# Kernel tuning notes

Hardware: AMD Instinct MI355X
Metric: run time of the kernel (lower is better)

Reference implementation:

```python
import jax, jax.numpy as jnp
import numpy as np

B, L, T = 256, 1024, 128


def setup_inputs() -> dict:
    key = jax.random.key(0)
    k1, k2, k3, k4 = jax.random.split(key, 4)
    inputs = jax.random.normal(k1, (B, L, T), dtype=jnp.float32)
    lengths = jax.random.randint(k2, (B,), 1, L + 1, dtype=jnp.int32)
    tags = jax.random.randint(k3, (B, L), 0, T, dtype=jnp.int32)
    # learned CRF transition matrix (random_normal_initializer default stddev=0.05)
    transition_params = jax.random.normal(k4, (T, T), dtype=jnp.float32) * 0.05
    return {"inputs": inputs, "lengths": lengths, "tags": tags,
            "transition_params": transition_params}


def _crf_decode(x, trans, lengths):
    """Viterbi decode. x: [B,L,T], trans: [T,T], lengths: [B] -> tags [B,L] int32."""
    Bx, Lx, Tx = x.shape

    def fwd_step(state, inp):
        x_t, t = inp  # x_t: [B,T]
        scores = state[:, :, None] + trans[None]          # [B, T_prev, T_cur]
        bp = jnp.argmax(scores, axis=1).astype(jnp.int32)  # [B,T]
        new_state = jnp.max(scores, axis=1) + x_t           # [B,T]
        m = (t < lengths)[:, None]
        state = jnp.where(m, new_state, state)
        bp = jnp.where(m, bp, 0)
        return state, bp

    init = x[:, 0]                                          # [B,T]
    xs = (jnp.swapaxes(x[:, 1:], 0, 1), jnp.arange(1, Lx))
    state, bps = jax.lax.scan(fwd_step, init, xs)           # bps: [L-1,B,T]
    bps = jnp.concatenate([jnp.zeros((1, Bx, Tx), jnp.int32), bps], axis=0)  # bp[0] unused
    last_tag = jnp.argmax(state, axis=-1).astype(jnp.int32)  # [B] tag at position length-1

    def bwd_step(carry, inp):
        bp_t, t = inp
        emit = jnp.where(t < lengths, carry, 0)             # tags beyond length -> 0
        prev = jnp.take_along_axis(bp_t, carry[:, None], axis=1)[:, 0]
        carry = jnp.where((t > 0) & (t < lengths), prev, carry)
        return carry, emit

    _, tags_rev = jax.lax.scan(bwd_step, last_tag, (bps[::-1], jnp.arange(Lx)[::-1]))
    return jnp.swapaxes(tags_rev[::-1], 0, 1)               # [B,L]


def reference(inputs, lengths, tags, transition_params):
    # Decoder.call: tfa.text.crf_decode(inputs, transition_params, lengths)[0]
    return _crf_decode(inputs, transition_params, lengths)
```

## Files before the change

kernel.cpp:

```cpp
#include <hip/hip_runtime.h>

#define BB 256
#define LL 1024
#define TT 128
#define NTH 512

__device__ __forceinline__ void lds_barrier() {
    asm volatile("s_waitcnt lgkmcnt(0)\n\ts_barrier" ::);
}

struct SmallSmem {
    float state[TT];
    float pv[NTH];
    int   pi[NTH];
    unsigned char tags[LL];
};

__global__ __launch_bounds__(NTH)
void viterbi_kernel(const float* __restrict__ x,
                    const int* __restrict__ lengths,
                    const float* __restrict__ trans,
                    int* __restrict__ out) {
    __shared__ SmallSmem sm;
    extern __shared__ unsigned char bp[];

    const int b   = blockIdx.x;
    const int tid = threadIdx.x;
    const int j   = tid & (TT - 1);
    const int q   = tid >> 7;

    int lenb = lengths[b];
    if (lenb < 1) lenb = 1;
    if (lenb > LL) lenb = LL;

    float tc[32];
    #pragma unroll
    for (int ii = 0; ii < 32; ++ii)
        tc[ii] = trans[(q * 32 + ii) * TT + j];

    const float* xb = x + (size_t)b * LL * TT;

    if (tid < TT) sm.state[tid] = xb[tid];

    float xv_cur = 0.0f, xv_next = 0.0f;
    if (tid < TT && lenb > 1) xv_cur = xb[TT + j];
    lds_barrier();

    for (int t = 1; t < lenb; ++t) {
        if (tid < TT) {
            int tn = (t + 1 < lenb) ? (t + 1) : (lenb - 1);
            xv_next = xb[tn * TT + j];
        }

        float best0 = -3.4e38f, best1 = -3.4e38f, best2 = -3.4e38f, best3 = -3.4e38f;
        int   bi0 = 0, bi1 = 1, bi2 = 2, bi3 = 3;
        const float4* st4 = reinterpret_cast<const float4*>(sm.state + q * 32);
        #pragma unroll
        for (int k = 0; k < 8; ++k) {
            float4 sv = st4[k];
            float s0 = sv.x + tc[4 * k + 0];
            float s1 = sv.y + tc[4 * k + 1];
            float s2 = sv.z + tc[4 * k + 2];
            float s3 = sv.w + tc[4 * k + 3];
            if (s0 > best0) { best0 = s0; bi0 = 4 * k + 0; }
            if (s1 > best1) { best1 = s1; bi1 = 4 * k + 1; }
            if (s2 > best2) { best2 = s2; bi2 = 4 * k + 2; }
            if (s3 > best3) { best3 = s3; bi3 = 4 * k + 3; }
        }
        float bb = best0; int bi = bi0;
        if (best1 > bb || (best1 == bb && bi1 < bi)) { bb = best1; bi = bi1; }
        if (best2 > bb || (best2 == bb && bi2 < bi)) { bb = best2; bi = bi2; }
        if (best3 > bb || (best3 == bb && bi3 < bi)) { bb = best3; bi = bi3; }
        sm.pv[tid] = bb;
        sm.pi[tid] = bi + q * 32;
        lds_barrier();

        if (tid < TT) {
            float bv = sm.pv[j];       int ix = sm.pi[j];
            float v1 = sm.pv[j + 128]; int i1 = sm.pi[j + 128];
            float v2 = sm.pv[j + 256]; int i2 = sm.pi[j + 256];
            float v3 = sm.pv[j + 384]; int i3 = sm.pi[j + 384];
            if (v1 > bv) { bv = v1; ix = i1; }
            if (v2 > bv) { bv = v2; ix = i2; }
            if (v3 > bv) { bv = v3; ix = i3; }
            sm.state[j] = bv + xv_cur;
            bp[t * TT + j] = (unsigned char)ix;
            xv_cur = xv_next;
        }
        lds_barrier();
    }

    if (tid == 0) {
        float bv = sm.state[0]; int ix = 0;
        for (int i = 1; i < TT; ++i) {
            float v = sm.state[i];
            if (v > bv) { bv = v; ix = i; }
        }
        int carry = ix;
        for (int t = lenb - 1; t >= 1; --t) {
            sm.tags[t] = (unsigned char)carry;
            carry = bp[t * TT + carry];
        }
        sm.tags[0] = (unsigned char)carry;
    }
    lds_barrier();

    int* outb = out + (size_t)b * LL;
    for (int t = tid; t < LL; t += NTH)
        outb[t] = (t < lenb) ? (int)sm.tags[t] : 0;
}

extern "C" void kernel_launch(void* const* d_in, const int* in_sizes, int n_in,
                              void* d_out, int out_size, void* d_ws, size_t ws_size,
                              hipStream_t stream) {
    const float* x       = (const float*)d_in[0];
    const int*   lengths = (const int*)d_in[1];
    const float* trans   = (const float*)d_in[3];
    int*         out     = (int*)d_out;

    const int dyn = LL * TT;
    hipFuncSetAttribute((const void*)&viterbi_kernel,
                        hipFuncAttributeMaxDynamicSharedMemorySize, dyn);
    viterbi_kernel<<<BB, NTH, dyn, stream>>>(x, lengths, trans, out);
}
```

Baseline: 934.1 us.

## Reduce Viterbi argmax across quad lanes with DPP and double-buffer state

Each output tag is now handled by four adjacent lanes, and their partial max/argmax results are combined with DPP quad permutes instead of going through shared memory. This removes one of the two block barriers per time step, along with the pv/pi shared-memory round trip. The state vector is double-buffered and padded so reads and writes of consecutive steps do not conflict. In exchange, every thread runs the shuffle compares, and the padded layout changes the LDS access pattern.

Result: slower. 984.3 us (+5.4%).

```diff
diff --git a/kernel.cpp b/kernel.cpp
--- a/kernel.cpp
+++ b/kernel.cpp
@@ -9,10 +9,21 @@
     asm volatile("s_waitcnt lgkmcnt(0)\n\ts_barrier" ::);
 }
 
-struct SmallSmem {
-    float state[TT];
-    float pv[NTH];
-    int   pi[NTH];
+template<int CTRL>
+__device__ __forceinline__ float dpp_f(float v) {
+    int r = __builtin_amdgcn_update_dpp(__float_as_int(v), __float_as_int(v),
+                                        CTRL, 0xF, 0xF, false);
+    return __int_as_float(r);
+}
+template<int CTRL>
+__device__ __forceinline__ int dpp_i(int v) {
+    return __builtin_amdgcn_update_dpp(v, v, CTRL, 0xF, 0xF, false);
+}
+
+#define SP(i) ((i) + (((i) >> 5) << 2))
+
+struct alignas(16) SmallSmem {
+    float st[2][144];
     unsigned char tags[LL];
 };
 
@@ -26,8 +37,8 @@
 
     const int b   = blockIdx.x;
     const int tid = threadIdx.x;
-    const int j   = tid & (TT - 1);
-    const int q   = tid >> 7;
+    const int j   = tid >> 2;
+    const int q   = tid & 3;
 
     int lenb = lengths[b];
     if (lenb < 1) lenb = 1;
@@ -40,21 +51,23 @@
 
     const float* xb = x + (size_t)b * LL * TT;
 
-    if (tid < TT) sm.state[tid] = xb[tid];
+    if (tid < TT) sm.st[0][SP(tid)] = xb[tid];
 
-    float xv_cur = 0.0f, xv_next = 0.0f;
-    if (tid < TT && lenb > 1) xv_cur = xb[TT + j];
+    float xv = 0.0f;
+    if (q == 0 && lenb > 1) xv = xb[TT + j];
     lds_barrier();
 
+    int p = 0;
     for (int t = 1; t < lenb; ++t) {
-        if (tid < TT) {
+        float xn = 0.0f;
+        if (q == 0) {
             int tn = (t + 1 < lenb) ? (t + 1) : (lenb - 1);
-            xv_next = xb[tn * TT + j];
+            xn = xb[tn * TT + j];
         }
 
+        const float4* st4 = reinterpret_cast<const float4*>(&sm.st[p][q * 36]);
         float best0 = -3.4e38f, best1 = -3.4e38f, best2 = -3.4e38f, best3 = -3.4e38f;
         int   bi0 = 0, bi1 = 1, bi2 = 2, bi3 = 3;
-        const float4* st4 = reinterpret_cast<const float4*>(sm.state + q * 32);
         #pragma unroll
         for (int k = 0; k < 8; ++k) {
             float4 sv = st4[k];
@@ -71,29 +84,30 @@
         if (best1 > bb || (best1 == bb && bi1 < bi)) { bb = best1; bi = bi1; }
         if (best2 > bb || (best2 == bb && bi2 < bi)) { bb = best2; bi = bi2; }
         if (best3 > bb || (best3 == bb && bi3 < bi)) { bb = best3; bi = bi3; }
-        sm.pv[tid] = bb;
-        sm.pi[tid] = bi + q * 32;
-        lds_barrier();
+        bi += q * 32;
 
-        if (tid < TT) {
-            float bv = sm.pv[j];       int ix = sm.pi[j];
-            float v1 = sm.pv[j + 128]; int i1 = sm.pi[j + 128];
-            float v2 = sm.pv[j + 256]; int i2 = sm.pi[j + 256];
-            float v3 = sm.pv[j + 384]; int i3 = sm.pi[j + 384];
-            if (v1 > bv) { bv = v1; ix = i1; }
-            if (v2 > bv) { bv = v2; ix = i2; }
-            if (v3 > bv) { bv = v3; ix = i3; }
-            sm.state[j] = bv + xv_cur;
-            bp[t * TT + j] = (unsigned char)ix;
-            xv_cur = xv_next;
+        {
+            float ov = dpp_f<0xB1>(bb);
+            int   oi = dpp_i<0xB1>(bi);
+            if (ov > bb || (ov == bb && oi < bi)) { bb = ov; bi = oi; }
+            ov = dpp_f<0x4E>(bb);
+            oi = dpp_i<0x4E>(bi);
+            if (ov > bb || (ov == bb && oi < bi)) { bb = ov; bi = oi; }
         }
+
+        if (q == 0) {
+            sm.st[p ^ 1][SP(j)] = bb + xv;
+            bp[t * TT + j] = (unsigned char)bi;
+            xv = xn;
+        }
+        p ^= 1;
         lds_barrier();
     }
 
     if (tid == 0) {
-        float bv = sm.state[0]; int ix = 0;
+        float bv = sm.st[p][SP(0)]; int ix = 0;
         for (int i = 1; i < TT; ++i) {
-            float v = sm.state[i];
+            float v = sm.st[p][SP(i)];
             if (v > bv) { bv = v; ix = i; }
         }
         int carry = ix;
```

## Drop argmax from forward pass; recover backpointers by recomputation during backtrace

Applied to the files above, without the earlier changes.

The forward Viterbi loop now computes only the max over previous states and writes each step's max value to a global workspace, so the per-step argmax bookkeeping and index reduction are gone. During backtrace, the chosen predecessor is found again by recomputing state+trans for the current tag and matching the stored max with a wavefront ballot. Workspace rows and inputs are staged into LDS in chunks. This adds a large global write stream (B*L*T floats) and a slower, serialized backward phase. Ties are resolved by taking the lowest matching index, and the recovered path relies on the recomputed float sums matching the stored maxima exactly.

Measured after the change: 776.1 us. -16.9%, faster.

```diff
diff --git a/kernel.cpp b/kernel.cpp
--- a/kernel.cpp
+++ b/kernel.cpp
@@ -4,9 +4,141 @@
 #define LL 1024
 #define TT 128
 #define NTH 512
+#define CH 64
+
+typedef unsigned long long ull;
 
 __device__ __forceinline__ void lds_barrier() {
     asm volatile("s_waitcnt lgkmcnt(0)\n\ts_barrier" ::);
+}
+
+struct FwdSmem {
+    float state[TT];
+    float pv[NTH];
+    unsigned char tags[LL];
+};
+
+__global__ __launch_bounds__(NTH)
+void viterbi_ws_kernel(const float* __restrict__ x,
+                       const int* __restrict__ lengths,
+                       const float* __restrict__ trans,
+                       int* __restrict__ out,
+                       float* __restrict__ ws) {
+    __shared__ FwdSmem sm;
+    extern __shared__ float dyn[];
+    float* tT = dyn;
+    float* bm = dyn + TT * TT;
+    float* bx = bm + CH * TT;
+
+    const int b   = blockIdx.x;
+    const int tid = threadIdx.x;
+    const int j   = tid & (TT - 1);
+    const int q   = tid >> 7;
+
+    int lenb = lengths[b];
+    if (lenb < 1) lenb = 1;
+    if (lenb > LL) lenb = LL;
+
+    float tc[32];
+    #pragma unroll
+    for (int ii = 0; ii < 32; ++ii) {
+        int r = q * 32 + ii;
+        float v = trans[r * TT + j];
+        tc[ii] = v;
+        tT[j * TT + r] = v;
+    }
+
+    const float* xb  = x  + (size_t)b * LL * TT;
+    float*       wsb = ws + (size_t)b * LL * TT;
+
+    if (tid < TT) { float v = xb[tid]; sm.state[tid] = v; wsb[tid] = v; }
+
+    float xv = 0.0f, xn = 0.0f;
+    if (tid < TT && lenb > 1) xv = xb[TT + j];
+    lds_barrier();
+
+    for (int t = 1; t < lenb; ++t) {
+        if (tid < TT) {
+            int tn = (t + 1 < lenb) ? (t + 1) : (lenb - 1);
+            xn = xb[tn * TT + j];
+        }
+        const float4* st4 = reinterpret_cast<const float4*>(sm.state + q * 32);
+        float m0 = -3.4e38f, m1 = -3.4e38f, m2 = -3.4e38f, m3 = -3.4e38f;
+        #pragma unroll
+        for (int k = 0; k < 8; ++k) {
+            float4 sv = st4[k];
+            m0 = fmaxf(m0, sv.x + tc[4 * k + 0]);
+            m1 = fmaxf(m1, sv.y + tc[4 * k + 1]);
+            m2 = fmaxf(m2, sv.z + tc[4 * k + 2]);
+            m3 = fmaxf(m3, sv.w + tc[4 * k + 3]);
+        }
+        sm.pv[tid] = fmaxf(fmaxf(m0, m1), fmaxf(m2, m3));
+        lds_barrier();
+        if (tid < TT) {
+            float bv = fmaxf(fmaxf(sm.pv[j], sm.pv[j + 128]),
+                             fmaxf(sm.pv[j + 256], sm.pv[j + 384]));
+            wsb[t * TT + j] = bv;
+            sm.state[j] = bv + xv;
+            xv = xn;
+        }
+        lds_barrier();
+    }
+
+    __syncthreads();
+
+    int c = 0; float mv = 0.0f;
+    const int l = tid;
+    if (tid < 64) {
+        float s0 = sm.state[l], s1 = sm.state[l + 64];
+        float mm = fmaxf(s0, s1);
+        #pragma unroll
+        for (int off = 1; off < 64; off <<= 1)
+            mm = fmaxf(mm, __shfl_xor(mm, off));
+        ull blo = __ballot(s0 == mm);
+        if (blo) c = __ffsll(blo) - 1;
+        else     c = 64 + __ffsll(__ballot(s1 == mm)) - 1;
+        if (lenb > 1) mv = wsb[(lenb - 1) * TT + c];
+    }
+
+    int rhi = lenb - 2;
+    while (rhi >= 0) {
+        int r0 = rhi - (CH - 1); if (r0 < 0) r0 = 0;
+        int nrows = rhi - r0 + 1;
+        const float4* wm4 = reinterpret_cast<const float4*>(wsb + r0 * TT);
+        const float4* wx4 = reinterpret_cast<const float4*>(xb  + r0 * TT);
+        float4* bm4 = reinterpret_cast<float4*>(bm);
+        float4* bx4 = reinterpret_cast<float4*>(bx);
+        int n4 = nrows * (TT / 4);
+        for (int i4 = tid; i4 < n4; i4 += NTH) {
+            bm4[i4] = wm4[i4];
+            float4 v = wx4[i4];
+            if (r0 == 0 && i4 < TT / 4) { v.x = 0.f; v.y = 0.f; v.z = 0.f; v.w = 0.f; }
+            bx4[i4] = v;
+        }
+        lds_barrier();
+        if (tid < 64) {
+            for (int t = r0 + nrows; t >= r0 + 1; --t) {
+                int row = (t - 1 - r0) * TT;
+                float slo = (bm[row + l]      + bx[row + l])      + tT[c * TT + l];
+                float shi = (bm[row + 64 + l] + bx[row + 64 + l]) + tT[c * TT + 64 + l];
+                ull blo = __ballot(slo == mv);
+                int nc;
+                if (blo) nc = __ffsll(blo) - 1;
+                else     nc = 64 + __ffsll(__ballot(shi == mv)) - 1;
+                if (l == 0) sm.tags[t] = (unsigned char)c;
+                c = nc;
+                mv = bm[row + c];
+            }
+        }
+        lds_barrier();
+        rhi = r0 - 1;
+    }
+    if (tid == 0) sm.tags[0] = (unsigned char)c;
+    lds_barrier();
+
+    int* outb = out + (size_t)b * LL;
+    for (int t = tid; t < LL; t += NTH)
+        outb[t] = (t < lenb) ? (int)sm.tags[t] : 0;
 }
 
 struct SmallSmem {
@@ -39,7 +171,6 @@
         tc[ii] = trans[(q * 32 + ii) * TT + j];
 
     const float* xb = x + (size_t)b * LL * TT;
-
     if (tid < TT) sm.state[tid] = xb[tid];
 
     float xv_cur = 0.0f, xv_next = 0.0f;
@@ -51,7 +182,6 @@
             int tn = (t + 1 < lenb) ? (t + 1) : (lenb - 1);
             xv_next = xb[tn * TT + j];
         }
-
         float best0 = -3.4e38f, best1 = -3.4e38f, best2 = -3.4e38f, best3 = -3.4e38f;
         int   bi0 = 0, bi1 = 1, bi2 = 2, bi3 = 3;
         const float4* st4 = reinterpret_cast<const float4*>(sm.state + q * 32);
@@ -118,8 +248,18 @@
     const float* trans   = (const float*)d_in[3];
     int*         out     = (int*)d_out;
 
-    const int dyn = LL * TT;
-    hipFuncSetAttribute((const void*)&viterbi_kernel,
-                        hipFuncAttributeMaxDynamicSharedMemorySize, dyn);
-    viterbi_kernel<<<BB, NTH, dyn, stream>>>(x, lengths, trans, out);
-}
+    const size_t ws_needed = (size_t)BB * LL * TT * sizeof(float);
+
+    if (d_ws != nullptr && ws_size >= ws_needed) {
+        const int dyn = (TT * TT + 2 * CH * TT) * (int)sizeof(float);
+        hipFuncSetAttribute((const void*)&viterbi_ws_kernel,
+                            hipFuncAttributeMaxDynamicSharedMemorySize, dyn);
+        viterbi_ws_kernel<<<BB, NTH, dyn, stream>>>(x, lengths, trans, out,
+                                                    (float*)d_ws);
+    } else {
+        const int dyn = LL * TT;
+        hipFuncSetAttribute((const void*)&viterbi_kernel,
+                            hipFuncAttributeMaxDynamicSharedMemorySize, dyn);
+        viterbi_kernel<<<BB, NTH, dyn, stream>>>(x, lengths, trans, out);
+    }
+}
```
